# Kernel tuning notes

Hardware: AMD Instinct MI355X
Metric: run time of the kernel (lower is better)

Reference implementation:

```python
import jax, jax.numpy as jnp
import numpy as np

N, G, E, F, H = 65536, 32768, 600000, 128, 128

def _mlp(x, w1, b1, w2, b2):
    # Linear -> SiLU -> Linear
    return jax.nn.silu(x @ w1 + b1) @ w2 + b2

def setup_inputs() -> dict:
    key = jax.random.key(0)
    ks = jax.random.split(key, 24)
    def lin(k, din, dout):
        kw, kb = jax.random.split(k)
        s = 1.0 / np.sqrt(din)
        return (jax.random.uniform(kw, (din, dout), jnp.float32, -s, s),
                jax.random.uniform(kb, (dout,), jnp.float32, -s, s))
    nm_w1, nm_b1 = lin(ks[0], F, H)
    nm_w2, nm_b2 = lin(ks[1], H, H)
    em_w1, em_b1 = lin(ks[2], 6, H)
    em_w2, em_b2 = lin(ks[3], H, H)
    mm_w1, mm_b1 = lin(ks[4], 2 * H, H)
    mm_w2, mm_b2 = lin(ks[5], H, H)
    um_w1, um_b1 = lin(ks[6], H, H)
    um_w2, um_b2 = lin(ks[7], H, H)
    return {
        "node_features": jax.random.normal(ks[8], (N, F), jnp.float32),
        "node_pos": jax.random.uniform(ks[9], (N, 3), jnp.float32),
        "grid_pos": jax.random.uniform(ks[10], (G, 3), jnp.float32),
        "edge_index": jax.random.randint(ks[11], (2, E), 0, G, jnp.int64),
        "nm_w1": nm_w1, "nm_b1": nm_b1, "nm_w2": nm_w2, "nm_b2": nm_b2,
        "em_w1": em_w1, "em_b1": em_b1, "em_w2": em_w2, "em_b2": em_b2,
        "mm_w1": mm_w1, "mm_b1": mm_b1, "mm_w2": mm_w2, "mm_b2": mm_b2,
        "um_w1": um_w1, "um_b1": um_b1, "um_w2": um_w2, "um_b2": um_b2,
    }

def reference(node_features, node_pos, grid_pos, edge_index,
              nm_w1, nm_b1, nm_w2, nm_b2,
              em_w1, em_b1, em_w2, em_b2,
              mm_w1, mm_b1, mm_w2, mm_b2,
              um_w1, um_b1, um_w2, um_b2):
    src, tgt = edge_index[0], edge_index[1]
    # node_model on all points [N,H]
    nf = _mlp(node_features, nm_w1, nm_b1, nm_w2, nm_b2)
    # edge features from gathered positions [E,6] -> [E,H]
    edge_attr = jnp.concatenate([node_pos[src], grid_pos[tgt]], axis=-1)
    ef = _mlp(edge_attr, em_w1, em_b1, em_w2, em_b2)
    # messages [E,2H] -> [E,H]
    msg = _mlp(jnp.concatenate([nf[src], ef], axis=-1), mm_w1, mm_b1, mm_w2, mm_b2)
    # scatter-add mean aggregation to grid [G,H]
    counts = jax.ops.segment_sum(jnp.ones((msg.shape[0],), msg.dtype), tgt, num_segments=G)
    counts = jnp.maximum(counts, 1.0)[:, None]
    agg = jax.ops.segment_sum(msg, tgt, num_segments=G) / counts
    # update_model [G,H]
    return _mlp(agg, um_w1, um_b1, um_w2, um_b2)
```

## Files before the change

### kernel.cpp

```cpp
#include <hip/hip_runtime.h>

#define N_NODES 65536
#define G_GRID  32768
#define E_EDGES 600000
#define HD      128

typedef __attribute__((ext_vector_type(8))) short bf8;
typedef __attribute__((ext_vector_type(4))) float f32x4;

__device__ __forceinline__ short f2bf(float f){
  union { float f; unsigned u; } v; v.f = f;
  unsigned r = v.u + 0x7FFFu + ((v.u >> 16) & 1u);
  return (short)(r >> 16);
}

__device__ __forceinline__ bf8 load_pack8(const float* p, float scale){
  float4 u0 = *(const float4*)p;
  float4 u1 = *(const float4*)(p + 4);
  bf8 r;
  r[0]=f2bf(u0.x*scale); r[1]=f2bf(u0.y*scale); r[2]=f2bf(u0.z*scale); r[3]=f2bf(u0.w*scale);
  r[4]=f2bf(u1.x*scale); r[5]=f2bf(u1.y*scale); r[6]=f2bf(u1.z*scale); r[7]=f2bf(u1.w*scale);
  return r;
}

__global__ void prep_w_k(const float* __restrict__ nmw1, const float* __restrict__ nmw2,
                         const float* __restrict__ emw2, const float* __restrict__ mmw1,
                         const float* __restrict__ mmw2, const float* __restrict__ umw1,
                         const float* __restrict__ umw2, short* __restrict__ dst)
{
  int i = blockIdx.x*256 + threadIdx.x;
  const float* src; int local; bool k256 = false;
  if      (i < 16384){ src = nmw1; local = i; }
  else if (i < 32768){ src = nmw2; local = i - 16384; }
  else if (i < 49152){ src = emw2; local = i - 32768; }
  else if (i < 81920){ src = mmw1; local = i - 49152; k256 = true; }
  else if (i < 98304){ src = mmw2; local = i - 81920; }
  else if (i < 114688){ src = umw1; local = i - 98304; }
  else               { src = umw2; local = i - 114688; }
  int n, k;
  if (k256){ n = local >> 8; k = local & 255; }
  else     { n = local >> 7; k = local & 127; }
  dst[i] = f2bf(src[k*HD + n]);
}

__global__ void prep_combo_k(const float* __restrict__ emw1, const float* __restrict__ eb1,
                             const float* __restrict__ emw2, const float* __restrict__ eb2,
                             const float* __restrict__ mmw1, const float* __restrict__ mb1,
                             short* __restrict__ wcombot, float* __restrict__ bcombo,
                             float* __restrict__ ew1c)
{
  int gid = blockIdx.x*256 + threadIdx.x;
  if (gid < 16384){
    int n = gid >> 7, k = gid & 127;
    float acc = 0.f;
    for (int j=0;j<HD;j++) acc += emw2[k*HD + j] * mmw1[(HD + j)*HD + n];
    wcombot[n*HD + k] = f2bf(acc);
  } else if (gid < 16512){
    int n = gid - 16384;
    float acc = mb1[n];
    for (int j=0;j<HD;j++) acc += eb2[j] * mmw1[(HD + j)*HD + n];
    bcombo[n] = acc;
  } else if (gid < 16640){
    int n = gid - 16512;
    #pragma unroll
    for (int k=0;k<6;k++) ew1c[n*8 + k] = emw1[k*HD + n];
    ew1c[n*8 + 6] = eb1[n];
    ew1c[n*8 + 7] = 0.f;
  }
}

__global__ void node_mlp_k(const float* __restrict__ X,
                           const short* __restrict__ w1t, const float* __restrict__ b1,
                           const short* __restrict__ w2t, const float* __restrict__ b2,
                           short* __restrict__ nf)
{
  __shared__ short hid[64][136];
  const int t = threadIdx.x;
  const int wave = t >> 6, lane = t & 63, l15 = lane & 15, q = lane >> 4;
  const int rw = blockIdx.x*64 + wave*16;

  bf8 a[4];
  const float* xr = X + (size_t)(rw + l15)*HD;
  #pragma unroll
  for (int kt=0; kt<4; kt++) a[kt] = load_pack8(xr + kt*32 + q*8, 1.0f);

  #pragma unroll
  for (int ct=0; ct<8; ct++){
    f32x4 acc = {0.f,0.f,0.f,0.f};
    #pragma unroll
    for (int kt=0; kt<4; kt++){
      bf8 b = *(const bf8*)(w1t + (ct*16 + l15)*HD + kt*32 + q*8);
      acc = __builtin_amdgcn_mfma_f32_16x16x32_bf16(a[kt], b, acc, 0, 0, 0);
    }
    float bias = b1[ct*16 + l15];
    #pragma unroll
    for (int r=0;r<4;r++){
      float v = acc[r] + bias;
      v = v / (1.f + __expf(-v));
      hid[wave*16 + q*4 + r][ct*16 + l15] = f2bf(v);
    }
  }
  __syncthreads();

  bf8 a2[4];
  #pragma unroll
  for (int kt=0;kt<4;kt++) a2[kt] = *(const bf8*)&hid[wave*16 + l15][kt*32 + q*8];
  #pragma unroll
  for (int ct=0; ct<8; ct++){
    f32x4 acc = {0.f,0.f,0.f,0.f};
    #pragma unroll
    for (int kt=0;kt<4;kt++){
      bf8 b = *(const bf8*)(w2t + (ct*16 + l15)*HD + kt*32 + q*8);
      acc = __builtin_amdgcn_mfma_f32_16x16x32_bf16(a2[kt], b, acc, 0, 0, 0);
    }
    float bias = b2[ct*16 + l15];
    #pragma unroll
    for (int r=0;r<4;r++)
      nf[(size_t)(rw + q*4 + r)*HD + ct*16 + l15] = f2bf(acc[r] + bias);
  }
}

__global__ void count_k(const int* __restrict__ eidx, int* __restrict__ counts){
  int e = blockIdx.x*256 + threadIdx.x;
  if (e < E_EDGES) atomicAdd(&counts[eidx[E_EDGES + e]], 1);
}

__global__ void scan_k(const int* __restrict__ counts, int* __restrict__ offs){
  __shared__ int part[1024];
  const int t = threadIdx.x;
  const int base = t*32;
  int loc[32];
  int s = 0;
  #pragma unroll
  for (int i=0;i<32;i++){ loc[i] = s; s += counts[base+i]; }
  part[t] = s;
  __syncthreads();
  for (int off=1; off<1024; off<<=1){
    int v = (t>=off) ? part[t-off] : 0;
    __syncthreads();
    part[t] += v;
    __syncthreads();
  }
  int pre = (t==0) ? 0 : part[t-1];
  #pragma unroll
  for (int i=0;i<32;i++) offs[base+i] = pre + loc[i];
  if (t==1023) offs[G_GRID] = pre + s;
}

__global__ void scatter_k(const int* __restrict__ eidx, const int* __restrict__ offs,
                          int* __restrict__ counts,
                          int* __restrict__ srcs_s, int* __restrict__ tgts_s){
  int e = blockIdx.x*256 + threadIdx.x;
  if (e < E_EDGES){
    int g = eidx[E_EDGES + e];
    int slot = offs[g] + atomicSub(&counts[g], 1) - 1;
    srcs_s[slot] = eidx[e];
    tgts_s[slot] = g;
  }
}

__global__ void __launch_bounds__(256, 3)
edge_msg2_k(const int* __restrict__ srcs_s, const int* __restrict__ tgts_s,
            const float* __restrict__ npos, const float* __restrict__ gpos,
            const float* __restrict__ ew1c_g, const float* __restrict__ bcombo,
            const short* __restrict__ mw1t, const short* __restrict__ wcombot,
            const short* __restrict__ mw2t, const float* __restrict__ mb2,
            const short* __restrict__ nf, float* __restrict__ agg)
{
  __shared__ float attr[128][9];
  __shared__ int tgtl[128];
  __shared__ float ew1l[128][8];
  union SmemU {
    short hm[128][136];
    float msgf[64][132];
  };
  __shared__ SmemU u;

  const int t = threadIdx.x;
  const int e0 = blockIdx.x*128;
  const int wave = t >> 6, lane = t & 63, l15 = lane & 15, q = lane >> 4;
  const int rl = wave*16;
  const bool v1 = (e0 + 64 < E_EDGES);

  int i0 = e0 + rl + l15;
  int i1 = e0 + 64 + rl + l15; if (i1 >= E_EDGES) i1 = E_EDGES - 1;
  int s0 = srcs_s[i0];
  int s1 = srcs_s[i1];

  bf8 an0[4], an1[4];
  {
    const short* n0p = nf + (size_t)s0*HD + q*8;
    const short* n1p = nf + (size_t)s1*HD + q*8;
    #pragma unroll
    for (int kt=0;kt<4;kt++){ an0[kt] = *(const bf8*)(n0p + kt*32); an1[kt] = *(const bf8*)(n1p + kt*32); }
  }

  if (t < 128){
    int idx = e0 + t; if (idx >= E_EDGES) idx = E_EDGES - 1;
    int s = srcs_s[idx], g = tgts_s[idx];
    tgtl[t] = g;
    attr[t][0] = npos[s*3+0]; attr[t][1] = npos[s*3+1]; attr[t][2] = npos[s*3+2];
    attr[t][3] = gpos[g*3+0]; attr[t][4] = gpos[g*3+1]; attr[t][5] = gpos[g*3+2];
  } else {
    int r = t - 128;
    *(f32x4*)&ew1l[r][0] = *(const f32x4*)&ew1c_g[r*8];
    *(f32x4*)&ew1l[r][4] = *(const f32x4*)&ew1c_g[r*8 + 4];
  }
  __syncthreads();

  {
    int e = t & 127, nb = (t >> 7)*64;
    float a0=attr[e][0], a1=attr[e][1], a2=attr[e][2],
          a3=attr[e][3], a4=attr[e][4], a5=attr[e][5];
    #pragma unroll
    for (int jg=0; jg<8; jg++){
      bf8 pk;
      #pragma unroll
      for (int j=0;j<8;j++){
        int n = nb + jg*8 + j;
        f32x4 w0 = *(const f32x4*)&ew1l[n][0];
        f32x4 w1 = *(const f32x4*)&ew1l[n][4];
        float v = w1[2] + a0*w0[0] + a1*w0[1] + a2*w0[2] + a3*w0[3] + a4*w1[0] + a5*w1[1];
        v = v / (1.f + __expf(-v));
        pk[j] = f2bf(v);
      }
      *(bf8*)&u.hm[e][nb + jg*8] = pk;
    }
  }
  __syncthreads();

  bf8 ah0[4], ah1[4];
  #pragma unroll
  for (int kt=0;kt<4;kt++){
    ah0[kt] = *(const bf8*)&u.hm[rl + l15][kt*32 + q*8];
    ah1[kt] = *(const bf8*)&u.hm[64 + rl + l15][kt*32 + q*8];
  }

  #pragma unroll
  for (int ct=0; ct<8; ct++){
    bf8 bw1[4], bwc[4];
    #pragma unroll
    for (int kt=0;kt<4;kt++){
      bw1[kt] = *(const bf8*)(mw1t + (ct*16 + l15)*256 + kt*32 + q*8);
      bwc[kt] = *(const bf8*)(wcombot + (ct*16 + l15)*HD + kt*32 + q*8);
    }
    f32x4 acc0 = {0.f,0.f,0.f,0.f}, acc1 = {0.f,0.f,0.f,0.f};
    #pragma unroll
    for (int kt=0;kt<4;kt++){
      acc0 = __builtin_amdgcn_mfma_f32_16x16x32_bf16(an0[kt], bw1[kt], acc0, 0,0,0);
      acc1 = __builtin_amdgcn_mfma_f32_16x16x32_bf16(an1[kt], bw1[kt], acc1, 0,0,0);
    }
    #pragma unroll
    for (int kt=0;kt<4;kt++){
      acc0 = __builtin_amdgcn_mfma_f32_16x16x32_bf16(ah0[kt], bwc[kt], acc0, 0,0,0);
      acc1 = __builtin_amdgcn_mfma_f32_16x16x32_bf16(ah1[kt], bwc[kt], acc1, 0,0,0);
    }
    float bias = bcombo[ct*16 + l15];
    int col = ct*16 + l15;
    #pragma unroll
    for (int r=0;r<4;r++){
      float v0 = acc0[r] + bias;
      v0 = v0 / (1.f + __expf(-v0));
      u.hm[rl + q*4 + r][col] = f2bf(v0);
      float v1f = acc1[r] + bias;
      v1f = v1f / (1.f + __expf(-v1f));
      u.hm[64 + rl + q*4 + r][col] = f2bf(v1f);
    }
  }

  bf8 am0[4], am1[4];
  #pragma unroll
  for (int kt=0;kt<4;kt++){
    am0[kt] = *(const bf8*)&u.hm[rl + l15][kt*32 + q*8];
    am1[kt] = *(const bf8*)&u.hm[64 + rl + l15][kt*32 + q*8];
  }
  __syncthreads();

  #pragma unroll
  for (int ct=0; ct<8; ct++){
    f32x4 acc = {0.f,0.f,0.f,0.f};
    #pragma unroll
    for (int kt=0;kt<4;kt++){
      bf8 b = *(const bf8*)(mw2t + (ct*16 + l15)*HD + kt*32 + q*8);
      acc = __builtin_amdgcn_mfma_f32_16x16x32_bf16(am0[kt], b, acc, 0,0,0);
    }
    float bias = mb2[ct*16 + l15];
    int col = ct*16 + l15;
    #pragma unroll
    for (int r=0;r<4;r++) u.msgf[rl + q*4 + r][col] = acc[r] + bias;
  }
  __syncthreads();
  {
    int col = t & 127, w = t >> 7;
    int base = w*32;
    int cur = tgtl[base];
    float sum = 0.f;
    for (int i=0;i<32;i++){
      int tg = tgtl[base+i];
      float v = u.msgf[base+i][col];
      if (tg != cur){ atomicAdd(&agg[(size_t)cur*HD + col], sum); cur = tg; sum = v; }
      else sum += v;
    }
    atomicAdd(&agg[(size_t)cur*HD + col], sum);
  }

  if (v1){
    __syncthreads();
    #pragma unroll
    for (int ct=0; ct<8; ct++){
      f32x4 acc = {0.f,0.f,0.f,0.f};
      #pragma unroll
      for (int kt=0;kt<4;kt++){
        bf8 b = *(const bf8*)(mw2t + (ct*16 + l15)*HD + kt*32 + q*8);
        acc = __builtin_amdgcn_mfma_f32_16x16x32_bf16(am1[kt], b, acc, 0,0,0);
      }
      float bias = mb2[ct*16 + l15];
      int col = ct*16 + l15;
      #pragma unroll
      for (int r=0;r<4;r++) u.msgf[rl + q*4 + r][col] = acc[r] + bias;
    }
    __syncthreads();
    {
      int col = t & 127, w = t >> 7;
      int base = w*32;
      int cur = tgtl[64 + base];
      float sum = 0.f;
      for (int i=0;i<32;i++){
        int tg = tgtl[64 + base+i];
        float v = u.msgf[base+i][col];
        if (tg != cur){ atomicAdd(&agg[(size_t)cur*HD + col], sum); cur = tg; sum = v; }
        else sum += v;
      }
      atomicAdd(&agg[(size_t)cur*HD + col], sum);
    }
  }
}

__global__ void update_mlp2_k(const float* __restrict__ agg, const int* __restrict__ offs,
                              const short* __restrict__ w1t, const float* __restrict__ b1,
                              const short* __restrict__ w2t, const float* __restrict__ b2,
                              float* __restrict__ out)
{
  __shared__ short hid[64][136];
  const int t = threadIdx.x;
  const int wave = t >> 6, lane = t & 63, l15 = lane & 15, q = lane >> 4;
  const int rw = blockIdx.x*64 + wave*16;

  int row = rw + l15;
  float c = (float)(offs[row+1] - offs[row]);
  float rcp = 1.0f / fmaxf(c, 1.0f);
  bf8 a[4];
  const float* ar = agg + (size_t)row*HD;
  #pragma unroll
  for (int kt=0; kt<4; kt++) a[kt] = load_pack8(ar + kt*32 + q*8, rcp);

  #pragma unroll
  for (int ct=0; ct<8; ct++){
    f32x4 acc = {0.f,0.f,0.f,0.f};
    #pragma unroll
    for (int kt=0; kt<4; kt++){
      bf8 b = *(const bf8*)(w1t + (ct*16 + l15)*HD + kt*32 + q*8);
      acc = __builtin_amdgcn_mfma_f32_16x16x32_bf16(a[kt], b, acc, 0, 0, 0);
    }
    float bias = b1[ct*16 + l15];
    #pragma unroll
    for (int r=0;r<4;r++){
      float v = acc[r] + bias;
      v = v / (1.f + __expf(-v));
      hid[wave*16 + q*4 + r][ct*16 + l15] = f2bf(v);
    }
  }
  __syncthreads();

  bf8 a2[4];
  #pragma unroll
  for (int kt=0;kt<4;kt++) a2[kt] = *(const bf8*)&hid[wave*16 + l15][kt*32 + q*8];
  #pragma unroll
  for (int ct=0; ct<8; ct++){
    f32x4 acc = {0.f,0.f,0.f,0.f};
    #pragma unroll
    for (int kt=0;kt<4;kt++){
      bf8 b = *(const bf8*)(w2t + (ct*16 + l15)*HD + kt*32 + q*8);
      acc = __builtin_amdgcn_mfma_f32_16x16x32_bf16(a2[kt], b, acc, 0, 0, 0);
    }
    float bias = b2[ct*16 + l15];
    #pragma unroll
    for (int r=0;r<4;r++)
      out[(size_t)(rw + q*4 + r)*HD + ct*16 + l15] = acc[r] + bias;
  }
}

extern "C" void kernel_launch(void* const* d_in, const int* in_sizes, int n_in,
                              void* d_out, int out_size, void* d_ws, size_t ws_size,
                              hipStream_t stream)
{
  const float* node_features = (const float*)d_in[0];
  const float* node_pos      = (const float*)d_in[1];
  const float* grid_pos      = (const float*)d_in[2];
  const int*   edge_index    = (const int*)d_in[3];
  const float* nm_w1 = (const float*)d_in[4];
  const float* nm_b1 = (const float*)d_in[5];
  const float* nm_w2 = (const float*)d_in[6];
  const float* nm_b2 = (const float*)d_in[7];
  const float* em_w1 = (const float*)d_in[8];
  const float* em_b1 = (const float*)d_in[9];
  const float* em_w2 = (const float*)d_in[10];
  const float* em_b2 = (const float*)d_in[11];
  const float* mm_w1 = (const float*)d_in[12];
  const float* mm_b1 = (const float*)d_in[13];
  const float* mm_w2 = (const float*)d_in[14];
  const float* mm_b2 = (const float*)d_in[15];
  const float* um_w1 = (const float*)d_in[16];
  const float* um_b1 = (const float*)d_in[17];
  const float* um_w2 = (const float*)d_in[18];
  const float* um_b2 = (const float*)d_in[19];
  float* out = (float*)d_out;

  char* ws = (char*)d_ws;
  short* nf     = (short*)ws;
  int*   counts = (int*)  (ws + 16777216ull);
  int*   offs   = (int*)  (ws + 16908288ull);
  short* wts    = (short*)(ws + 17039424ull);
  short* wcombot= (short*)(ws + 17301568ull);
  float* bcombo = (float*)(ws + 17334336ull);
  float* ew1c   = (float*)(ws + 17334848ull);
  int*   srcs_s = (int*)  (ws + 17338944ull);
  int*   tgts_s = (int*)  (ws + 19738944ull);

  short* nmw1t = wts;
  short* nmw2t = wts + 16384;
  short* mmw1t = wts + 49152;
  short* mmw2t = wts + 81920;
  short* umw1t = wts + 98304;
  short* umw2t = wts + 114688;

  float* agg = out;

  (void)hipMemsetAsync(counts, 0, 131072, stream);
  (void)hipMemsetAsync(out, 0, (size_t)G_GRID*HD*4, stream);

  prep_w_k<<<512, 256, 0, stream>>>(nm_w1, nm_w2, em_w2, mm_w1, mm_w2, um_w1, um_w2, wts);
  prep_combo_k<<<65, 256, 0, stream>>>(em_w1, em_b1, em_w2, em_b2, mm_w1, mm_b1,
                                       wcombot, bcombo, ew1c);
  node_mlp_k<<<N_NODES/64, 256, 0, stream>>>(node_features, nmw1t, nm_b1, nmw2t, nm_b2, nf);
  count_k<<<(E_EDGES+255)/256, 256, 0, stream>>>(edge_index, counts);
  scan_k<<<1, 1024, 0, stream>>>(counts, offs);
  scatter_k<<<(E_EDGES+255)/256, 256, 0, stream>>>(edge_index, offs, counts, srcs_s, tgts_s);
  edge_msg2_k<<<(E_EDGES + 127)/128, 256, 0, stream>>>(srcs_s, tgts_s, node_pos, grid_pos,
      ew1c, bcombo, mmw1t, wcombot, mmw2t, mm_b2, nf, agg);
  update_mlp2_k<<<G_GRID/64, 256, 0, stream>>>(agg, offs, umw1t, um_b1, umw2t, um_b2, out);
}
```

Measured before the change: 556.7 us.

## Make edge message kernel wave-private to drop block barriers and raise occupancy

The edge kernel now gives each wave its own 32 contiguous edges and a private shared-memory arena. The first edge-MLP layer is computed directly into MFMA operand registers, which removes the shared staging buffer and most __syncthreads calls. Segmented atomic reduction now runs per wave with float2 columns. Launch bounds are raised to 4 blocks per SM and shared memory is smaller, to improve occupancy. Separately, the intra-wave barriers are removed in the node and update MLPs, and the prep weight-combo loop is reordered for coalescing. The cost is redundant per-lane edge-MLP work (each lane computes 32 hidden units for 2 edges) and more register pressure.

```diff
diff --git a/kernel.cpp b/kernel.cpp
--- a/kernel.cpp
+++ b/kernel.cpp
@@ -51,10 +51,14 @@
 {
   int gid = blockIdx.x*256 + threadIdx.x;
   if (gid < 16384){
-    int n = gid >> 7, k = gid & 127;
-    float acc = 0.f;
-    for (int j=0;j<HD;j++) acc += emw2[k*HD + j] * mmw1[(HD + j)*HD + n];
-    wcombot[n*HD + k] = f2bf(acc);
+    int k = gid >> 7, n = gid & 127;
+    float a0 = 0.f, a1 = 0.f;
+    #pragma unroll 4
+    for (int j=0;j<HD;j+=2){
+      a0 += emw2[k*HD + j]     * mmw1[(HD + j)*HD + n];
+      a1 += emw2[k*HD + j + 1] * mmw1[(HD + j + 1)*HD + n];
+    }
+    wcombot[n*HD + k] = f2bf(a0 + a1);
   } else if (gid < 16512){
     int n = gid - 16384;
     float acc = mb1[n];
@@ -100,8 +104,6 @@
       hid[wave*16 + q*4 + r][ct*16 + l15] = f2bf(v);
     }
   }
-  __syncthreads();
-
   bf8 a2[4];
   #pragma unroll
   for (int kt=0;kt<4;kt++) a2[kt] = *(const bf8*)&hid[wave*16 + l15][kt*32 + q*8];
@@ -159,33 +161,31 @@
   }
 }
 
-__global__ void __launch_bounds__(256, 3)
-edge_msg2_k(const int* __restrict__ srcs_s, const int* __restrict__ tgts_s,
+__global__ void __launch_bounds__(256, 4)
+edge_msg3_k(const int* __restrict__ srcs_s, const int* __restrict__ tgts_s,
             const float* __restrict__ npos, const float* __restrict__ gpos,
             const float* __restrict__ ew1c_g, const float* __restrict__ bcombo,
             const short* __restrict__ mw1t, const short* __restrict__ wcombot,
             const short* __restrict__ mw2t, const float* __restrict__ mb2,
             const short* __restrict__ nf, float* __restrict__ agg)
 {
-  __shared__ float attr[128][9];
+  __shared__ float ew1l[128][8];
   __shared__ int tgtl[128];
-  __shared__ float ew1l[128][8];
-  union SmemU {
-    short hm[128][136];
-    float msgf[64][132];
+  union WArena {
+    short hm[32][136];
+    float msgf[16][132];
   };
-  __shared__ SmemU u;
+  __shared__ WArena ar[4];
 
   const int t = threadIdx.x;
   const int e0 = blockIdx.x*128;
-  const int wave = t >> 6, lane = t & 63, l15 = lane & 15, q = lane >> 4;
-  const int rl = wave*16;
-  const bool v1 = (e0 + 64 < E_EDGES);
-
-  int i0 = e0 + rl + l15;
-  int i1 = e0 + 64 + rl + l15; if (i1 >= E_EDGES) i1 = E_EDGES - 1;
-  int s0 = srcs_s[i0];
-  int s1 = srcs_s[i1];
+  const int w = t >> 6, lane = t & 63, l15 = lane & 15, q = lane >> 4;
+  const int base = e0 + w*32;
+
+  int i0 = base + l15;      if (i0 >= E_EDGES) i0 = E_EDGES - 1;
+  int i1 = base + 16 + l15; if (i1 >= E_EDGES) i1 = E_EDGES - 1;
+  int s0 = srcs_s[i0], s1 = srcs_s[i1];
+  int g0 = tgts_s[i0], g1 = tgts_s[i1];
 
   bf8 an0[4], an1[4];
   {
@@ -194,46 +194,37 @@
     #pragma unroll
     for (int kt=0;kt<4;kt++){ an0[kt] = *(const bf8*)(n0p + kt*32); an1[kt] = *(const bf8*)(n1p + kt*32); }
   }
+  float p0[6], p1[6];
+  p0[0]=npos[s0*3+0]; p0[1]=npos[s0*3+1]; p0[2]=npos[s0*3+2];
+  p0[3]=gpos[g0*3+0]; p0[4]=gpos[g0*3+1]; p0[5]=gpos[g0*3+2];
+  p1[0]=npos[s1*3+0]; p1[1]=npos[s1*3+1]; p1[2]=npos[s1*3+2];
+  p1[3]=gpos[g1*3+0]; p1[4]=gpos[g1*3+1]; p1[5]=gpos[g1*3+2];
 
   if (t < 128){
     int idx = e0 + t; if (idx >= E_EDGES) idx = E_EDGES - 1;
-    int s = srcs_s[idx], g = tgts_s[idx];
-    tgtl[t] = g;
-    attr[t][0] = npos[s*3+0]; attr[t][1] = npos[s*3+1]; attr[t][2] = npos[s*3+2];
-    attr[t][3] = gpos[g*3+0]; attr[t][4] = gpos[g*3+1]; attr[t][5] = gpos[g*3+2];
-  } else {
-    int r = t - 128;
-    *(f32x4*)&ew1l[r][0] = *(const f32x4*)&ew1c_g[r*8];
-    *(f32x4*)&ew1l[r][4] = *(const f32x4*)&ew1c_g[r*8 + 4];
+    tgtl[t] = tgts_s[idx];
+    *(f32x4*)&ew1l[t][0] = *(const f32x4*)&ew1c_g[t*8];
+    *(f32x4*)&ew1l[t][4] = *(const f32x4*)&ew1c_g[t*8 + 4];
   }
   __syncthreads();
 
-  {
-    int e = t & 127, nb = (t >> 7)*64;
-    float a0=attr[e][0], a1=attr[e][1], a2=attr[e][2],
-          a3=attr[e][3], a4=attr[e][4], a5=attr[e][5];
-    #pragma unroll
-    for (int jg=0; jg<8; jg++){
-      bf8 pk;
-      #pragma unroll
-      for (int j=0;j<8;j++){
-        int n = nb + jg*8 + j;
-        f32x4 w0 = *(const f32x4*)&ew1l[n][0];
-        f32x4 w1 = *(const f32x4*)&ew1l[n][4];
-        float v = w1[2] + a0*w0[0] + a1*w0[1] + a2*w0[2] + a3*w0[3] + a4*w1[0] + a5*w1[1];
-        v = v / (1.f + __expf(-v));
-        pk[j] = f2bf(v);
-      }
-      *(bf8*)&u.hm[e][nb + jg*8] = pk;
-    }
-  }
-  __syncthreads();
-
   bf8 ah0[4], ah1[4];
   #pragma unroll
   for (int kt=0;kt<4;kt++){
-    ah0[kt] = *(const bf8*)&u.hm[rl + l15][kt*32 + q*8];
-    ah1[kt] = *(const bf8*)&u.hm[64 + rl + l15][kt*32 + q*8];
+    #pragma unroll
+    for (int j=0;j<8;j++){
+      int n = kt*32 + q*8 + j;
+      f32x4 wa = *(const f32x4*)&ew1l[n][0];
+      f32x4 wb = *(const f32x4*)&ew1l[n][4];
+      float v0 = wb[2] + p0[0]*wa[0] + p0[1]*wa[1] + p0[2]*wa[2]
+                       + p0[3]*wa[3] + p0[4]*wb[0] + p0[5]*wb[1];
+      v0 = v0 / (1.f + __expf(-v0));
+      ah0[kt][j] = f2bf(v0);
+      float v1 = wb[2] + p1[0]*wa[0] + p1[1]*wa[1] + p1[2]*wa[2]
+                       + p1[3]*wa[3] + p1[4]*wb[0] + p1[5]*wb[1];
+      v1 = v1 / (1.f + __expf(-v1));
+      ah1[kt][j] = f2bf(v1);
+    }
   }
 
   #pragma unroll
@@ -261,20 +252,19 @@
     for (int r=0;r<4;r++){
       float v0 = acc0[r] + bias;
       v0 = v0 / (1.f + __expf(-v0));
-      u.hm[rl + q*4 + r][col] = f2bf(v0);
-      float v1f = acc1[r] + bias;
-      v1f = v1f / (1.f + __expf(-v1f));
-      u.hm[64 + rl + q*4 + r][col] = f2bf(v1f);
+      ar[w].hm[q*4 + r][col] = f2bf(v0);
+      float v1 = acc1[r] + bias;
+      v1 = v1 / (1.f + __expf(-v1));
+      ar[w].hm[16 + q*4 + r][col] = f2bf(v1);
     }
   }
 
   bf8 am0[4], am1[4];
   #pragma unroll
   for (int kt=0;kt<4;kt++){
-    am0[kt] = *(const bf8*)&u.hm[rl + l15][kt*32 + q*8];
-    am1[kt] = *(const bf8*)&u.hm[64 + rl + l15][kt*32 + q*8];
-  }
-  __syncthreads();
+    am0[kt] = *(const bf8*)&ar[w].hm[l15][kt*32 + q*8];
+    am1[kt] = *(const bf8*)&ar[w].hm[16 + l15][kt*32 + q*8];
+  }
 
   #pragma unroll
   for (int ct=0; ct<8; ct++){
@@ -287,25 +277,29 @@
     float bias = mb2[ct*16 + l15];
     int col = ct*16 + l15;
     #pragma unroll
-    for (int r=0;r<4;r++) u.msgf[rl + q*4 + r][col] = acc[r] + bias;
-  }
-  __syncthreads();
+    for (int r=0;r<4;r++) ar[w].msgf[q*4 + r][col] = acc[r] + bias;
+  }
   {
-    int col = t & 127, w = t >> 7;
-    int base = w*32;
-    int cur = tgtl[base];
-    float sum = 0.f;
-    for (int i=0;i<32;i++){
-      int tg = tgtl[base+i];
-      float v = u.msgf[base+i][col];
-      if (tg != cur){ atomicAdd(&agg[(size_t)cur*HD + col], sum); cur = tg; sum = v; }
-      else sum += v;
-    }
-    atomicAdd(&agg[(size_t)cur*HD + col], sum);
-  }
-
-  if (v1){
-    __syncthreads();
+    int lim = E_EDGES - base; if (lim > 16) lim = 16;
+    if (lim > 0){
+      int c2 = lane*2;
+      int cur = tgtl[w*32];
+      float sx = 0.f, sy = 0.f;
+      for (int r=0; r<lim; r++){
+        int tg = tgtl[w*32 + r];
+        float2 v = *(const float2*)&ar[w].msgf[r][c2];
+        if (tg != cur){
+          atomicAdd(&agg[(size_t)cur*HD + c2], sx);
+          atomicAdd(&agg[(size_t)cur*HD + c2 + 1], sy);
+          cur = tg; sx = v.x; sy = v.y;
+        } else { sx += v.x; sy += v.y; }
+      }
+      atomicAdd(&agg[(size_t)cur*HD + c2], sx);
+      atomicAdd(&agg[(size_t)cur*HD + c2 + 1], sy);
+    }
+  }
+
+  if (base + 16 < E_EDGES){
     #pragma unroll
     for (int ct=0; ct<8; ct++){
       f32x4 acc = {0.f,0.f,0.f,0.f};
@@ -317,22 +311,23 @@
       float bias = mb2[ct*16 + l15];
       int col = ct*16 + l15;
       #pragma unroll
-      for (int r=0;r<4;r++) u.msgf[rl + q*4 + r][col] = acc[r] + bias;
-    }
-    __syncthreads();
-    {
-      int col = t & 127, w = t >> 7;
-      int base = w*32;
-      int cur = tgtl[64 + base];
-      float sum = 0.f;
-      for (int i=0;i<32;i++){
-        int tg = tgtl[64 + base+i];
-        float v = u.msgf[base+i][col];
-        if (tg != cur){ atomicAdd(&agg[(size_t)cur*HD + col], sum); cur = tg; sum = v; }
-        else sum += v;
-      }
-      atomicAdd(&agg[(size_t)cur*HD + col], sum);
-    }
+      for (int r=0;r<4;r++) ar[w].msgf[q*4 + r][col] = acc[r] + bias;
+    }
+    int lim = E_EDGES - (base + 16); if (lim > 16) lim = 16;
+    int c2 = lane*2;
+    int cur = tgtl[w*32 + 16];
+    float sx = 0.f, sy = 0.f;
+    for (int r=0; r<lim; r++){
+      int tg = tgtl[w*32 + 16 + r];
+      float2 v = *(const float2*)&ar[w].msgf[r][c2];
+      if (tg != cur){
+        atomicAdd(&agg[(size_t)cur*HD + c2], sx);
+        atomicAdd(&agg[(size_t)cur*HD + c2 + 1], sy);
+        cur = tg; sx = v.x; sy = v.y;
+      } else { sx += v.x; sy += v.y; }
+    }
+    atomicAdd(&agg[(size_t)cur*HD + c2], sx);
+    atomicAdd(&agg[(size_t)cur*HD + c2 + 1], sy);
   }
 }
 
@@ -370,8 +365,6 @@
       hid[wave*16 + q*4 + r][ct*16 + l15] = f2bf(v);
     }
   }
-  __syncthreads();
-
   bf8 a2[4];
   #pragma unroll
   for (int kt=0;kt<4;kt++) a2[kt] = *(const bf8*)&hid[wave*16 + l15][kt*32 + q*8];
@@ -446,7 +439,7 @@
   count_k<<<(E_EDGES+255)/256, 256, 0, stream>>>(edge_index, counts);
   scan_k<<<1, 1024, 0, stream>>>(counts, offs);
   scatter_k<<<(E_EDGES+255)/256, 256, 0, stream>>>(edge_index, offs, counts, srcs_s, tgts_s);
-  edge_msg2_k<<<(E_EDGES + 127)/128, 256, 0, stream>>>(srcs_s, tgts_s, node_pos, grid_pos,
+  edge_msg3_k<<<(E_EDGES + 127)/128, 256, 0, stream>>>(srcs_s, tgts_s, node_pos, grid_pos,
       ew1c, bcombo, mmw1t, wcombot, mmw2t, mm_b2, nf, agg);
   update_mlp2_k<<<G_GRID/64, 256, 0, stream>>>(agg, offs, umw1t, um_b1, umw2t, um_b2, out);
 }
```

Result: slower. 605.2 us (+8.7%).
